# Kernel optimization log

Measured on AMD Instinct MI355X. Metric: run time of the kernel, lower is better.

## Reference

```python
import jax, jax.numpy as jnp
import numpy as np

B, S, C = 2, 2048, 512
L, H, CH = 4, 8, 64  # layers, heads, per-head channel (H*CH == C)
OD = 4 * CH          # GEGLU output_dim = channel*4 = 256
EPS = 1e-5


def layer_norm(x, g, b):
    mu = jnp.mean(x, axis=-1, keepdims=True)
    var = jnp.mean(jnp.square(x - mu), axis=-1, keepdims=True)
    return (x - mu) * jax.lax.rsqrt(var + EPS) * g + b


def gelu_tanh(g):
    # matches: 0.5 * g * (1 + tanh(g * 0.7978845608 * (1 + 0.044715 * g**2)))
    t = jnp.tanh(g * 0.7978845608 * (1.0 + 0.044715 * jnp.square(g)))
    return 0.5 * g * (1.0 + t)


def setup_inputs() -> dict:
    key = jax.random.key(0)
    ks = jax.random.split(key, 8)
    s = 0.02
    return {
        "x": jax.random.normal(ks[0], (B, S, C), jnp.float32),
        "ln_gamma": jnp.ones((L + 1, C), jnp.float32),
        "ln_beta": jnp.zeros((L + 1, C), jnp.float32),
        "Wq": jax.random.normal(ks[1], (L, C, H * CH), jnp.float32) * s,
        "Wk": jax.random.normal(ks[2], (L, C, H * CH), jnp.float32) * s,
        "Wv": jax.random.normal(ks[3], (L, C, H * CH), jnp.float32) * s,
        "Wo": jax.random.normal(ks[4], (L, H * CH, C), jnp.float32) * s,
        "bo": jnp.zeros((L, C), jnp.float32),
        "Wg": jax.random.normal(ks[5], (C, 2 * OD), jnp.float32) * s,
        "bg": jnp.zeros((2 * OD,), jnp.float32),
        "Wf": jax.random.normal(ks[6], (OD, C), jnp.float32) * s,
        "bf": jnp.zeros((C,), jnp.float32),
    }


def reference(x, ln_gamma, ln_beta, Wq, Wk, Wv, Wo, bo, Wg, bg, Wf, bf):
    scale = 1.0 / jnp.sqrt(jnp.asarray(CH, x.dtype))
    for i in range(L):
        h = layer_norm(x, ln_gamma[i], ln_beta[i])
        q = (h @ Wq[i]).reshape(B, S, H, CH)
        k = (h @ Wk[i]).reshape(B, S, H, CH)
        v = (h @ Wv[i]).reshape(B, S, H, CH)
        scores = jnp.einsum("bqhc,bkhc->bhqk", q, k) * scale
        w = jax.nn.softmax(scores, axis=-1)
        o = jnp.einsum("bhqk,bkhc->bqhc", w, v).reshape(B, S, H * CH)
        x = o @ Wo[i] + bo[i] + x
    h = layer_norm(x, ln_gamma[L], ln_beta[L])
    g = h @ Wg + bg
    a, gate = g[..., :OD], g[..., OD:]
    ff = a * gelu_tanh(gate)
    return ff @ Wf + bf + x
```

## Files before the change

### kernel.cpp

```cpp
#include <hip/hip_runtime.h>
#include <hip/hip_bf16.h>


typedef __bf16 bf16_t;
typedef __attribute__((ext_vector_type(8))) __bf16 bf16x8;
typedef __attribute__((ext_vector_type(4))) __bf16 bf16x4;
typedef __attribute__((ext_vector_type(4))) float f32x4;

#define MROWS 4096

static __device__ __forceinline__ void gload_lds16(const void* g, void* l) {
  __builtin_amdgcn_global_load_lds((const __attribute__((address_space(1))) void*)g,
                                   (__attribute__((address_space(3))) void*)l, 16, 0, 0);
}

__global__ __launch_bounds__(256) void ln_kernel(const float* __restrict__ xin,
    const float* __restrict__ gamma, const float* __restrict__ beta,
    bf16_t* __restrict__ hout)
{
  int w = threadIdx.x >> 6, l = threadIdx.x & 63;
  int row = blockIdx.x * 4 + w;
  const float* xr = xin + (size_t)row * 512 + l * 8;
  f32x4 a = *(const f32x4*)xr;
  f32x4 b2 = *(const f32x4*)(xr + 4);
  float s = a[0]+a[1]+a[2]+a[3]+b2[0]+b2[1]+b2[2]+b2[3];
  #pragma unroll
  for (int m = 1; m < 64; m <<= 1) s += __shfl_xor(s, m, 64);
  float mu = s * (1.0f/512.0f);
  float vs = 0.f;
  #pragma unroll
  for (int i = 0; i < 4; i++) { float d = a[i]-mu; vs += d*d; d = b2[i]-mu; vs += d*d; }
  #pragma unroll
  for (int m = 1; m < 64; m <<= 1) vs += __shfl_xor(vs, m, 64);
  float rstd = rsqrtf(vs * (1.0f/512.0f) + 1e-5f);
  const float* gp = gamma + l*8;
  const float* bp = beta + l*8;
  f32x4 g0 = *(const f32x4*)gp, g1 = *(const f32x4*)(gp+4);
  f32x4 p0 = *(const f32x4*)bp, p1 = *(const f32x4*)(bp+4);
  bf16x8 h;
  #pragma unroll
  for (int i = 0; i < 4; i++) {
    h[i]   = (bf16_t)((a[i]-mu)*rstd*g0[i] + p0[i]);
    h[4+i] = (bf16_t)((b2[i]-mu)*rstd*g1[i] + p1[i]);
  }
  *(bf16x8*)(hout + (size_t)row*512 + l*8) = h;
}

__global__ __launch_bounds__(256) void prep_kernel(
    const float* __restrict__ Wq, const float* __restrict__ Wk, const float* __restrict__ Wv,
    const float* __restrict__ Wo, const float* __restrict__ Wg, const float* __restrict__ Wf,
    bf16_t* __restrict__ WqkvT, bf16_t* __restrict__ WoT,
    bf16_t* __restrict__ WgT, bf16_t* __restrict__ WfT)
{
  __shared__ float tile[32][33];
  int z = blockIdx.z;
  const float* src; bf16_t* dst; int K = 512, N = 512;
  if (z < 12) {
    int lay = z & 3, which = z >> 2;
    src = (which == 0 ? Wq : which == 1 ? Wk : Wv) + (size_t)lay*512*512;
    dst = WqkvT + (size_t)lay*1536*512 + (size_t)which*512*512;
  } else if (z < 16) {
    src = Wo + (size_t)(z-12)*512*512;
    dst = WoT + (size_t)(z-12)*512*512;
  } else if (z == 16) { src = Wg; dst = WgT; }
  else { src = Wf; dst = WfT; K = 256; }
  int k0 = blockIdx.y*32, n0 = blockIdx.x*32;
  if (k0 >= K) return;
  int tx = threadIdx.x & 31, ty = threadIdx.x >> 5;
  #pragma unroll
  for (int j = 0; j < 4; j++)
    tile[ty + j*8][tx] = src[(size_t)(k0 + ty + j*8)*N + n0 + tx];
  __syncthreads();
  #pragma unroll
  for (int j = 0; j < 4; j++)
    dst[(size_t)(n0 + ty + j*8)*K + k0 + tx] = (bf16_t)tile[tx][ty + j*8];
}

template<int EPI>
__global__ __launch_bounds__(256) void gemm_bt(
    const bf16_t* __restrict__ A, const bf16_t* __restrict__ Bt,
    int N, int K,
    void* __restrict__ Cout, bf16_t* __restrict__ vTout,
    const float* __restrict__ bias, const float* __restrict__ resid, float qscale)
{
  __shared__ bf16_t As[128*64];
  __shared__ bf16_t Bs[128*64];
  int t = threadIdx.x, w = t >> 6, l = t & 63;
  int tm = blockIdx.y * 128, tn = blockIdx.x * 128;
  int wm = (w >> 1) * 64, wn = (w & 1) * 64;
  f32x4 acc[4][4] = {};
  int srow = l >> 3;
  int schunk = ((l & 7) ^ srow) * 8;
  for (int k0 = 0; k0 < K; k0 += 64) {
    __syncthreads();
    #pragma unroll
    for (int i = 0; i < 4; i++) {
      int rb = i*32 + w*8;
      gload_lds16(A  + (size_t)(tm + rb + srow)*K + k0 + schunk, &As[rb*64]);
      gload_lds16(Bt + (size_t)(tn + rb + srow)*K + k0 + schunk, &Bs[rb*64]);
    }
    __syncthreads();
    #pragma unroll
    for (int kk = 0; kk < 2; kk++) {
      bf16x8 af[4], bfr[4];
      #pragma unroll
      for (int mf = 0; mf < 4; mf++) {
        int row = wm + mf*16 + (l & 15);
        int off = (kk*32 + (l >> 4)*8) ^ ((row & 7) << 3);
        af[mf] = *(const bf16x8*)&As[row*64 + off];
      }
      #pragma unroll
      for (int nf = 0; nf < 4; nf++) {
        int row = wn + nf*16 + (l & 15);
        int off = (kk*32 + (l >> 4)*8) ^ ((row & 7) << 3);
        bfr[nf] = *(const bf16x8*)&Bs[row*64 + off];
      }
      #pragma unroll
      for (int mf = 0; mf < 4; mf++)
        #pragma unroll
        for (int nf = 0; nf < 4; nf++)
          acc[mf][nf] = __builtin_amdgcn_mfma_f32_16x16x32_bf16(af[mf], bfr[nf], acc[mf][nf], 0, 0, 0);
    }
  }
  int colb = tn + wn + (l & 15);
  int rowb = tm + wm + ((l >> 4) << 2);
  if (EPI == 0 && tn >= 1024) {
    #pragma unroll
    for (int mf = 0; mf < 4; mf++)
      #pragma unroll
      for (int nf = 0; nf < 4; nf++) {
        int col = colb + nf*16;
        int hh = (col - 1024) >> 6, ch = (col - 1024) & 63;
        int row = rowb + mf*16;
        int bb = row >> 11, sdx = row & 2047;
        bf16x4 pk;
        #pragma unroll
        for (int r = 0; r < 4; r++) pk[r] = (bf16_t)acc[mf][nf][r];
        *(bf16x4*)&vTout[(((size_t)bb*8 + hh)*64 + ch)*2048 + sdx] = pk;
      }
    return;
  }
  #pragma unroll
  for (int mf = 0; mf < 4; mf++)
    #pragma unroll
    for (int nf = 0; nf < 4; nf++)
      #pragma unroll
      for (int r = 0; r < 4; r++) {
        int row = rowb + mf*16 + r;
        int col = colb + nf*16;
        float v = acc[mf][nf][r];
        if (EPI == 0) {
          if (col < 512) v *= qscale;
          ((bf16_t*)Cout)[(size_t)row*1024 + col] = (bf16_t)v;
        } else if (EPI == 1) {
          ((float*)Cout)[(size_t)row*N + col] = v + bias[col] + resid[(size_t)row*N + col];
        } else {
          ((float*)Cout)[(size_t)row*N + col] = v + bias[col];
        }
      }
}

__global__ __launch_bounds__(256) void attn_kernel(const bf16_t* __restrict__ qkv,
                                                   const bf16_t* __restrict__ vT,
                                                   bf16_t* __restrict__ obuf)
{
  __shared__ bf16_t Qs[64*64];
  __shared__ bf16_t Ks[2][64*64];
  __shared__ bf16_t Vs[2][64*64];
  __shared__ bf16_t Ps[4*16*72];
  int t = threadIdx.x, w = t >> 6, l = t & 63;
  int q0 = blockIdx.x * 64, h = blockIdx.y, b = blockIdx.z;
  size_t rbase = (size_t)b * 2048;
  int srow = l >> 3;
  int schunk = ((l & 7) ^ srow) * 8;
  int rb0 = w*16, rb1 = w*16 + 8;
  const bf16_t* qb = qkv + (rbase + q0) * 1024 + h*64;
  gload_lds16(qb + (size_t)(rb0 + srow)*1024 + schunk, &Qs[rb0*64]);
  gload_lds16(qb + (size_t)(rb1 + srow)*1024 + schunk, &Qs[rb1*64]);
  const bf16_t* kb  = qkv + rbase*1024 + 512 + h*64;
  const bf16_t* vtb = vT + ((size_t)(b*8 + h)*64)*2048;
  gload_lds16(kb + (size_t)(rb0 + srow)*1024 + schunk, &Ks[0][rb0*64]);
  gload_lds16(kb + (size_t)(rb1 + srow)*1024 + schunk, &Ks[0][rb1*64]);
  gload_lds16(vtb + (size_t)(rb0 + srow)*2048 + schunk, &Vs[0][rb0*64]);
  gload_lds16(vtb + (size_t)(rb1 + srow)*2048 + schunk, &Vs[0][rb1*64]);

  int lq = l & 15, hi = l >> 4;
  int pw = w * 16 * 72;
  f32x4 accO[4] = {};
  f32x4 lacc = {};
  bf16x8 aq[2];
  bf16x8 ones;
  #pragma unroll
  for (int e = 0; e < 8; e++) ones[e] = (bf16_t)1.0f;
  int qrow = w*16 + lq;
  int swz = (lq & 7) << 3;

  for (int tt = 0; tt < 32; ++tt) {
    int cur = tt & 1;
    if (tt < 31) {
      int kv1 = (tt + 1) * 64;
      int nxt = cur ^ 1;
      gload_lds16(kb + (size_t)(kv1 + rb0 + srow)*1024 + schunk, &Ks[nxt][rb0*64]);
      gload_lds16(kb + (size_t)(kv1 + rb1 + srow)*1024 + schunk, &Ks[nxt][rb1*64]);
      gload_lds16(vtb + (size_t)(rb0 + srow)*2048 + kv1 + schunk, &Vs[nxt][rb0*64]);
      gload_lds16(vtb + (size_t)(rb1 + srow)*2048 + kv1 + schunk, &Vs[nxt][rb1*64]);
      asm volatile("s_waitcnt vmcnt(4)" ::: "memory");
    } else {
      asm volatile("s_waitcnt vmcnt(0)" ::: "memory");
    }
    __builtin_amdgcn_s_barrier();
    if (tt == 0) {
      aq[0] = *(const bf16x8*)&Qs[qrow*64 + ((hi*8) ^ swz)];
      aq[1] = *(const bf16x8*)&Qs[qrow*64 + ((32 + hi*8) ^ swz)];
    }
    f32x4 s4[4] = {};
    #pragma unroll
    for (int kk = 0; kk < 2; kk++) {
      int off = (kk*32 + hi*8) ^ swz;
      #pragma unroll
      for (int nf = 0; nf < 4; nf++) {
        bf16x8 bk = *(const bf16x8*)&Ks[cur][(nf*16 + lq)*64 + off];
        s4[nf] = __builtin_amdgcn_mfma_f32_16x16x32_bf16(aq[kk], bk, s4[nf], 0, 0, 0);
      }
    }
    #pragma unroll
    for (int nf = 0; nf < 4; nf++)
      #pragma unroll
      for (int r = 0; r < 4; r++)
        Ps[pw + (hi*4 + r)*72 + nf*16 + lq] = (bf16_t)exp2f(s4[nf][r]);
    #pragma unroll
    for (int kk = 0; kk < 2; kk++) {
      int off = (kk*32 + hi*8) ^ swz;
      bf16x8 pa = *(const bf16x8*)&Ps[pw + lq*72 + kk*32 + hi*8];
      lacc = __builtin_amdgcn_mfma_f32_16x16x32_bf16(pa, ones, lacc, 0, 0, 0);
      #pragma unroll
      for (int nf = 0; nf < 4; nf++) {
        bf16x8 vv = *(const bf16x8*)&Vs[cur][(nf*16 + lq)*64 + off];
        accO[nf] = __builtin_amdgcn_mfma_f32_16x16x32_bf16(pa, vv, accO[nf], 0, 0, 0);
      }
    }
    asm volatile("s_waitcnt lgkmcnt(0)" ::: "memory");
    __builtin_amdgcn_s_barrier();
  }
  f32x4 linv;
  #pragma unroll
  for (int r = 0; r < 4; r++) linv[r] = 1.0f / lacc[r];
  size_t orow = rbase + q0 + w*16 + hi*4;
  #pragma unroll
  for (int nf = 0; nf < 4; nf++)
    #pragma unroll
    for (int r = 0; r < 4; r++)
      obuf[(orow + r)*512 + h*64 + nf*16 + lq] = (bf16_t)(accO[nf][r] * linv[r]);
}

__global__ __launch_bounds__(256) void gelu_kernel(const float* __restrict__ g,
                                                   bf16_t* __restrict__ ff)
{
  int idx = blockIdx.x * 256 + threadIdx.x;
  int row = idx >> 6;
  int c = (idx & 63) * 4;
  const float* gr = g + (size_t)row*512;
  f32x4 a = *(const f32x4*)(gr + c);
  f32x4 u = *(const f32x4*)(gr + 256 + c);
  bf16x4 o4;
  #pragma unroll
  for (int i = 0; i < 4; i++) {
    float x = u[i];
    float tt = tanhf(0.7978845608f * x * (1.0f + 0.044715f * x * x));
    o4[i] = (bf16_t)(a[i] * 0.5f * x * (1.0f + tt));
  }
  *(bf16x4*)(ff + (size_t)row*256 + c) = o4;
}

extern "C" void kernel_launch(void* const* d_in, const int* in_sizes, int n_in,
                              void* d_out, int out_size, void* d_ws, size_t ws_size,
                              hipStream_t stream)
{
  const float* x     = (const float*)d_in[0];
  const float* gamma = (const float*)d_in[1];
  const float* beta  = (const float*)d_in[2];
  const float* Wq    = (const float*)d_in[3];
  const float* Wk    = (const float*)d_in[4];
  const float* Wv    = (const float*)d_in[5];
  const float* Wo    = (const float*)d_in[6];
  const float* bo    = (const float*)d_in[7];
  const float* Wg    = (const float*)d_in[8];
  const float* bg    = (const float*)d_in[9];
  const float* Wf    = (const float*)d_in[10];
  const float* bf    = (const float*)d_in[11];

  char* ws = (char*)d_ws;
  float*  xcur  = (float*)ws;
  bf16_t* hbuf  = (bf16_t*)(ws + (8u<<20));
  bf16_t* qkv   = (bf16_t*)(ws + (12u<<20));
  bf16_t* vT    = (bf16_t*)(ws + (20u<<20));
  bf16_t* obuf  = (bf16_t*)(ws + (24u<<20));
  bf16_t* WqkvT = (bf16_t*)(ws + (28u<<20));
  bf16_t* WoT   = (bf16_t*)(ws + (34u<<20));
  bf16_t* WgT   = (bf16_t*)(ws + (36u<<20));
  bf16_t* WfT   = (bf16_t*)(ws + (36u<<20) + (512u<<10));
  float*  gbuf  = (float*)qkv;
  bf16_t* ffb   = obuf;

  const float QSCALE = 0.125f * 1.44269504f;

  prep_kernel<<<dim3(16,16,18), 256, 0, stream>>>(Wq,Wk,Wv,Wo,Wg,Wf,WqkvT,WoT,WgT,WfT);
  hipMemcpyAsync(xcur, x, (size_t)MROWS*512*4, hipMemcpyDeviceToDevice, stream);

  for (int lay = 0; lay < 4; lay++) {
    ln_kernel<<<1024, 256, 0, stream>>>(xcur, gamma + lay*512, beta + lay*512, hbuf);
    gemm_bt<0><<<dim3(12,32), 256, 0, stream>>>(hbuf, WqkvT + (size_t)lay*1536*512,
                                                1536, 512, qkv, vT, nullptr, nullptr, QSCALE);
    attn_kernel<<<dim3(32,8,2), 256, 0, stream>>>(qkv, vT, obuf);
    gemm_bt<1><<<dim3(4,32), 256, 0, stream>>>(obuf, WoT + (size_t)lay*512*512,
                                               512, 512, xcur, nullptr, bo + lay*512, xcur, 1.0f);
  }
  ln_kernel<<<1024, 256, 0, stream>>>(xcur, gamma + 4*512, beta + 4*512, hbuf);
  gemm_bt<2><<<dim3(4,32), 256, 0, stream>>>(hbuf, WgT, 512, 512, gbuf, nullptr, bg, nullptr, 1.0f);
  gelu_kernel<<<1024, 256, 0, stream>>>(gbuf, ffb);
  gemm_bt<1><<<dim3(4,32), 256, 0, stream>>>(ffb, WfT, 512, 256, d_out, nullptr, bf, xcur, 1.0f);
}
```

Before: 442.6 us.

## Split attention over KV halves with combine kernel, shrink GEMM M-tile

Attention is split into two KV halves per query block, which doubles the grid. Each half writes unnormalised fp32 partial outputs and row sums, and a new combine kernel adds them and normalises. Q and V fragments now load straight into registers instead of through LDS, and exp2 uses the raw v_exp_f32 instruction. The GEMMs are templated on BM and launched with 64-row tiles to get more blocks on the many CUs. The cost is an extra kernel launch plus fp32 partial-output traffic, and lower per-block reuse in the GEMMs.

Result: slower. 516.0 us (+16.6%).

```diff
diff --git a/kernel.cpp b/kernel.cpp
--- a/kernel.cpp
+++ b/kernel.cpp
@@ -8,10 +8,17 @@
 typedef __attribute__((ext_vector_type(4))) float f32x4;
 
 #define MROWS 4096
+#define KVSPLIT 2
+#define NT 16
 
 static __device__ __forceinline__ void gload_lds16(const void* g, void* l) {
   __builtin_amdgcn_global_load_lds((const __attribute__((address_space(1))) void*)g,
                                    (__attribute__((address_space(3))) void*)l, 16, 0, 0);
+}
+static __device__ __forceinline__ float fexp2(float x) {
+  float r;
+  asm("v_exp_f32 %0, %1" : "=v"(r) : "v"(x));
+  return r;
 }
 
 __global__ __launch_bounds__(256) void ln_kernel(const float* __restrict__ xin,
@@ -76,35 +83,40 @@
     dst[(size_t)(n0 + ty + j*8)*K + k0 + tx] = (bf16_t)tile[tx][ty + j*8];
 }
 
-template<int EPI>
+template<int EPI, int BM>
 __global__ __launch_bounds__(256) void gemm_bt(
     const bf16_t* __restrict__ A, const bf16_t* __restrict__ Bt,
     int N, int K,
     void* __restrict__ Cout, bf16_t* __restrict__ vTout,
     const float* __restrict__ bias, const float* __restrict__ resid, float qscale)
 {
-  __shared__ bf16_t As[128*64];
+  __shared__ bf16_t As[BM*64];
   __shared__ bf16_t Bs[128*64];
+  constexpr int MF = BM/32;
   int t = threadIdx.x, w = t >> 6, l = t & 63;
-  int tm = blockIdx.y * 128, tn = blockIdx.x * 128;
-  int wm = (w >> 1) * 64, wn = (w & 1) * 64;
-  f32x4 acc[4][4] = {};
+  int tm = blockIdx.y * BM, tn = blockIdx.x * 128;
+  int wm = (w >> 1) * (BM/2), wn = (w & 1) * 64;
+  f32x4 acc[MF][4] = {};
   int srow = l >> 3;
   int schunk = ((l & 7) ^ srow) * 8;
   for (int k0 = 0; k0 < K; k0 += 64) {
     __syncthreads();
     #pragma unroll
+    for (int i = 0; i < BM/32; i++) {
+      int rb = i*32 + w*8;
+      gload_lds16(A + (size_t)(tm + rb + srow)*K + k0 + schunk, &As[rb*64]);
+    }
+    #pragma unroll
     for (int i = 0; i < 4; i++) {
       int rb = i*32 + w*8;
-      gload_lds16(A  + (size_t)(tm + rb + srow)*K + k0 + schunk, &As[rb*64]);
       gload_lds16(Bt + (size_t)(tn + rb + srow)*K + k0 + schunk, &Bs[rb*64]);
     }
     __syncthreads();
     #pragma unroll
     for (int kk = 0; kk < 2; kk++) {
-      bf16x8 af[4], bfr[4];
-      #pragma unroll
-      for (int mf = 0; mf < 4; mf++) {
+      bf16x8 af[MF], bfr[4];
+      #pragma unroll
+      for (int mf = 0; mf < MF; mf++) {
         int row = wm + mf*16 + (l & 15);
         int off = (kk*32 + (l >> 4)*8) ^ ((row & 7) << 3);
         af[mf] = *(const bf16x8*)&As[row*64 + off];
@@ -116,7 +128,7 @@
         bfr[nf] = *(const bf16x8*)&Bs[row*64 + off];
       }
       #pragma unroll
-      for (int mf = 0; mf < 4; mf++)
+      for (int mf = 0; mf < MF; mf++)
         #pragma unroll
         for (int nf = 0; nf < 4; nf++)
           acc[mf][nf] = __builtin_amdgcn_mfma_f32_16x16x32_bf16(af[mf], bfr[nf], acc[mf][nf], 0, 0, 0);
@@ -126,7 +138,7 @@
   int rowb = tm + wm + ((l >> 4) << 2);
   if (EPI == 0 && tn >= 1024) {
     #pragma unroll
-    for (int mf = 0; mf < 4; mf++)
+    for (int mf = 0; mf < MF; mf++)
       #pragma unroll
       for (int nf = 0; nf < 4; nf++) {
         int col = colb + nf*16;
@@ -141,7 +153,7 @@
     return;
   }
   #pragma unroll
-  for (int mf = 0; mf < 4; mf++)
+  for (int mf = 0; mf < MF; mf++)
     #pragma unroll
     for (int nf = 0; nf < 4; nf++)
       #pragma unroll
@@ -162,95 +174,119 @@
 
 __global__ __launch_bounds__(256) void attn_kernel(const bf16_t* __restrict__ qkv,
                                                    const bf16_t* __restrict__ vT,
-                                                   bf16_t* __restrict__ obuf)
-{
-  __shared__ bf16_t Qs[64*64];
+                                                   float* __restrict__ Ows,
+                                                   float* __restrict__ lws)
+{
   __shared__ bf16_t Ks[2][64*64];
-  __shared__ bf16_t Vs[2][64*64];
   __shared__ bf16_t Ps[4*16*72];
   int t = threadIdx.x, w = t >> 6, l = t & 63;
-  int q0 = blockIdx.x * 64, h = blockIdx.y, b = blockIdx.z;
+  int q0 = blockIdx.x * 64, h = blockIdx.y;
+  int b = blockIdx.z >> 1, sp = blockIdx.z & 1;
   size_t rbase = (size_t)b * 2048;
+  int kvb = sp * (2048/KVSPLIT);
+  int lq = l & 15, hi = l >> 4;
   int srow = l >> 3;
   int schunk = ((l & 7) ^ srow) * 8;
   int rb0 = w*16, rb1 = w*16 + 8;
-  const bf16_t* qb = qkv + (rbase + q0) * 1024 + h*64;
-  gload_lds16(qb + (size_t)(rb0 + srow)*1024 + schunk, &Qs[rb0*64]);
-  gload_lds16(qb + (size_t)(rb1 + srow)*1024 + schunk, &Qs[rb1*64]);
   const bf16_t* kb  = qkv + rbase*1024 + 512 + h*64;
-  const bf16_t* vtb = vT + ((size_t)(b*8 + h)*64)*2048;
-  gload_lds16(kb + (size_t)(rb0 + srow)*1024 + schunk, &Ks[0][rb0*64]);
-  gload_lds16(kb + (size_t)(rb1 + srow)*1024 + schunk, &Ks[0][rb1*64]);
-  gload_lds16(vtb + (size_t)(rb0 + srow)*2048 + schunk, &Vs[0][rb0*64]);
-  gload_lds16(vtb + (size_t)(rb1 + srow)*2048 + schunk, &Vs[0][rb1*64]);
-
-  int lq = l & 15, hi = l >> 4;
+  const bf16_t* vtb = vT + ((size_t)(b*8 + h)*64)*2048 + kvb;
+  const bf16_t* qp = qkv + (rbase + q0 + w*16 + lq)*1024 + h*64 + hi*8;
+  bf16x8 aq0 = *(const bf16x8*)qp;
+  bf16x8 aq1 = *(const bf16x8*)(qp + 32);
+  const bf16_t* vp = vtb + (size_t)lq*2048 + hi*8;
+
+  gload_lds16(kb + (size_t)(kvb + rb0 + srow)*1024 + schunk, &Ks[0][rb0*64]);
+  gload_lds16(kb + (size_t)(kvb + rb1 + srow)*1024 + schunk, &Ks[0][rb1*64]);
+  bf16x8 vv[8];
+  #pragma unroll
+  for (int kk = 0; kk < 2; kk++)
+    #pragma unroll
+    for (int nf = 0; nf < 4; nf++)
+      vv[kk*4+nf] = *(const bf16x8*)(vp + (size_t)nf*16*2048 + kk*32);
+  asm volatile("s_waitcnt vmcnt(8)" ::: "memory");
+  __builtin_amdgcn_s_barrier();
+
   int pw = w * 16 * 72;
   f32x4 accO[4] = {};
   f32x4 lacc = {};
-  bf16x8 aq[2];
   bf16x8 ones;
   #pragma unroll
   for (int e = 0; e < 8; e++) ones[e] = (bf16_t)1.0f;
-  int qrow = w*16 + lq;
   int swz = (lq & 7) << 3;
 
-  for (int tt = 0; tt < 32; ++tt) {
+  for (int tt = 0; tt < NT; ++tt) {
     int cur = tt & 1;
-    if (tt < 31) {
-      int kv1 = (tt + 1) * 64;
-      int nxt = cur ^ 1;
-      gload_lds16(kb + (size_t)(kv1 + rb0 + srow)*1024 + schunk, &Ks[nxt][rb0*64]);
-      gload_lds16(kb + (size_t)(kv1 + rb1 + srow)*1024 + schunk, &Ks[nxt][rb1*64]);
-      gload_lds16(vtb + (size_t)(rb0 + srow)*2048 + kv1 + schunk, &Vs[nxt][rb0*64]);
-      gload_lds16(vtb + (size_t)(rb1 + srow)*2048 + kv1 + schunk, &Vs[nxt][rb1*64]);
-      asm volatile("s_waitcnt vmcnt(4)" ::: "memory");
-    } else {
-      asm volatile("s_waitcnt vmcnt(0)" ::: "memory");
-    }
-    __builtin_amdgcn_s_barrier();
-    if (tt == 0) {
-      aq[0] = *(const bf16x8*)&Qs[qrow*64 + ((hi*8) ^ swz)];
-      aq[1] = *(const bf16x8*)&Qs[qrow*64 + ((32 + hi*8) ^ swz)];
+    if (tt < NT-1) {
+      int kv1 = kvb + (tt + 1) * 64;
+      gload_lds16(kb + (size_t)(kv1 + rb0 + srow)*1024 + schunk, &Ks[cur^1][rb0*64]);
+      gload_lds16(kb + (size_t)(kv1 + rb1 + srow)*1024 + schunk, &Ks[cur^1][rb1*64]);
     }
     f32x4 s4[4] = {};
     #pragma unroll
     for (int kk = 0; kk < 2; kk++) {
       int off = (kk*32 + hi*8) ^ swz;
+      bf16x8 aq = kk ? aq1 : aq0;
       #pragma unroll
       for (int nf = 0; nf < 4; nf++) {
         bf16x8 bk = *(const bf16x8*)&Ks[cur][(nf*16 + lq)*64 + off];
-        s4[nf] = __builtin_amdgcn_mfma_f32_16x16x32_bf16(aq[kk], bk, s4[nf], 0, 0, 0);
+        s4[nf] = __builtin_amdgcn_mfma_f32_16x16x32_bf16(aq, bk, s4[nf], 0, 0, 0);
       }
     }
     #pragma unroll
     for (int nf = 0; nf < 4; nf++)
       #pragma unroll
       for (int r = 0; r < 4; r++)
-        Ps[pw + (hi*4 + r)*72 + nf*16 + lq] = (bf16_t)exp2f(s4[nf][r]);
+        Ps[pw + (hi*4 + r)*72 + nf*16 + lq] = (bf16_t)fexp2(s4[nf][r]);
+    if (tt < NT-1) asm volatile("s_waitcnt vmcnt(2)" ::: "memory");
+    else           asm volatile("s_waitcnt vmcnt(0)" ::: "memory");
     #pragma unroll
     for (int kk = 0; kk < 2; kk++) {
-      int off = (kk*32 + hi*8) ^ swz;
       bf16x8 pa = *(const bf16x8*)&Ps[pw + lq*72 + kk*32 + hi*8];
       lacc = __builtin_amdgcn_mfma_f32_16x16x32_bf16(pa, ones, lacc, 0, 0, 0);
       #pragma unroll
-      for (int nf = 0; nf < 4; nf++) {
-        bf16x8 vv = *(const bf16x8*)&Vs[cur][(nf*16 + lq)*64 + off];
-        accO[nf] = __builtin_amdgcn_mfma_f32_16x16x32_bf16(pa, vv, accO[nf], 0, 0, 0);
-      }
+      for (int nf = 0; nf < 4; nf++)
+        accO[nf] = __builtin_amdgcn_mfma_f32_16x16x32_bf16(pa, vv[kk*4+nf], accO[nf], 0, 0, 0);
+    }
+    if (tt < NT-1) {
+      const bf16_t* vn = vp + (tt + 1) * 64;
+      #pragma unroll
+      for (int kk = 0; kk < 2; kk++)
+        #pragma unroll
+        for (int nf = 0; nf < 4; nf++)
+          vv[kk*4+nf] = *(const bf16x8*)(vn + (size_t)nf*16*2048 + kk*32);
     }
     asm volatile("s_waitcnt lgkmcnt(0)" ::: "memory");
+    asm volatile("s_waitcnt vmcnt(8)" ::: "memory");
     __builtin_amdgcn_s_barrier();
   }
-  f32x4 linv;
-  #pragma unroll
-  for (int r = 0; r < 4; r++) linv[r] = 1.0f / lacc[r];
-  size_t orow = rbase + q0 + w*16 + hi*4;
+  float* op = Ows + (size_t)sp*MROWS*512 + (rbase + q0 + w*16 + hi*4)*512 + h*64 + lq;
   #pragma unroll
   for (int nf = 0; nf < 4; nf++)
     #pragma unroll
     for (int r = 0; r < 4; r++)
-      obuf[(orow + r)*512 + h*64 + nf*16 + lq] = (bf16_t)(accO[nf][r] * linv[r]);
+      op[(size_t)r*512 + nf*16] = accO[nf][r];
+  if (lq == 0) {
+    size_t rowb = rbase + q0 + w*16 + hi*4;
+    #pragma unroll
+    for (int r = 0; r < 4; r++)
+      lws[(size_t)sp*MROWS*8 + (rowb + r)*8 + h] = lacc[r];
+  }
+}
+
+__global__ __launch_bounds__(256) void combine_kernel(const float* __restrict__ Ows,
+                                                      const float* __restrict__ lws,
+                                                      bf16_t* __restrict__ obuf)
+{
+  int idx = blockIdx.x * 256 + threadIdx.x;
+  int row = idx >> 7, c4 = (idx & 127) * 4;
+  f32x4 o0 = *(const f32x4*)&Ows[(size_t)row*512 + c4];
+  f32x4 o1 = *(const f32x4*)&Ows[(size_t)(MROWS + row)*512 + c4];
+  int h = c4 >> 6;
+  float li = 1.0f / (lws[row*8 + h] + lws[MROWS*8 + row*8 + h]);
+  bf16x4 o;
+  #pragma unroll
+  for (int i = 0; i < 4; i++) o[i] = (bf16_t)((o0[i] + o1[i]) * li);
+  *(bf16x4*)&obuf[(size_t)row*512 + c4] = o;
 }
 
 __global__ __launch_bounds__(256) void gelu_kernel(const float* __restrict__ g,
@@ -299,6 +335,8 @@
   bf16_t* WoT   = (bf16_t*)(ws + (34u<<20));
   bf16_t* WgT   = (bf16_t*)(ws + (36u<<20));
   bf16_t* WfT   = (bf16_t*)(ws + (36u<<20) + (512u<<10));
+  float*  lws   = (float*)(ws + (37u<<20));
+  float*  Ows   = (float*)(ws + (40u<<20));
   float*  gbuf  = (float*)qkv;
   bf16_t* ffb   = obuf;
 
@@ -309,14 +347,15 @@
 
   for (int lay = 0; lay < 4; lay++) {
     ln_kernel<<<1024, 256, 0, stream>>>(xcur, gamma + lay*512, beta + lay*512, hbuf);
-    gemm_bt<0><<<dim3(12,32), 256, 0, stream>>>(hbuf, WqkvT + (size_t)lay*1536*512,
-                                                1536, 512, qkv, vT, nullptr, nullptr, QSCALE);
-    attn_kernel<<<dim3(32,8,2), 256, 0, stream>>>(qkv, vT, obuf);
-    gemm_bt<1><<<dim3(4,32), 256, 0, stream>>>(obuf, WoT + (size_t)lay*512*512,
-                                               512, 512, xcur, nullptr, bo + lay*512, xcur, 1.0f);
+    gemm_bt<0,64><<<dim3(12,64), 256, 0, stream>>>(hbuf, WqkvT + (size_t)lay*1536*512,
+                                                   1536, 512, qkv, vT, nullptr, nullptr, QSCALE);
+    attn_kernel<<<dim3(32,8,2*KVSPLIT), 256, 0, stream>>>(qkv, vT, Ows, lws);
+    combine_kernel<<<2048, 256, 0, stream>>>(Ows, lws, obuf);
+    gemm_bt<1,64><<<dim3(4,64), 256, 0, stream>>>(obuf, WoT + (size_t)lay*512*512,
+                                                  512, 512, xcur, nullptr, bo + lay*512, xcur, 1.0f);
   }
   ln_kernel<<<1024, 256, 0, stream>>>(xcur, gamma + 4*512, beta + 4*512, hbuf);
-  gemm_bt<2><<<dim3(4,32), 256, 0, stream>>>(hbuf, WgT, 512, 512, gbuf, nullptr, bg, nullptr, 1.0f);
+  gemm_bt<2,64><<<dim3(4,64), 256, 0, stream>>>(hbuf, WgT, 512, 512, gbuf, nullptr, bg, nullptr, 1.0f);
   gelu_kernel<<<1024, 256, 0, stream>>>(gbuf, ffb);
-  gemm_bt<1><<<dim3(4,32), 256, 0, stream>>>(ffb, WfT, 512, 256, d_out, nullptr, bf, xcur, 1.0f);
-}
+  gemm_bt<1,64><<<dim3(4,64), 256, 0, stream>>>(ffb, WfT, 512, 256, d_out, nullptr, bf, xcur, 1.0f);
+}
```
